# Performance work log

Hardware: AMD Instinct MI355X
Metric: run time of the kernel (lower is better)

The kernel has to match this reference:

```python
import jax, jax.numpy as jnp
import numpy as np

N_NODES = 50000
N_EDGES = 1_600_000
D = 256
H = 8
HD = D // H
EDGE_DIM = 32


def layer_norm(x, g, b, eps=1e-5):
    mu = jnp.mean(x, axis=-1, keepdims=True)
    var = jnp.var(x, axis=-1, keepdims=True)
    return (x - mu) * jax.lax.rsqrt(var + eps) * g + b


def setup_inputs() -> dict:
    key = jax.random.key(0)
    ks = jax.random.split(key, 24)
    def lin(k, out_d, in_d):
        s = 1.0 / np.sqrt(in_d)
        kw, kb = jax.random.split(k)
        W = jax.random.uniform(kw, (out_d, in_d), jnp.float32, -s, s)
        b = jax.random.uniform(kb, (out_d,), jnp.float32, -s, s)
        return W, b
    Wq, bq = lin(ks[0], D, D)
    Wk, bk = lin(ks[1], D, D)
    Wv, bv = lin(ks[2], D, D)
    We, be = lin(ks[3], HD, EDGE_DIM)
    Wo, bo = lin(ks[4], D, D)
    W1, b1 = lin(ks[5], 4 * D, D)
    W2, b2 = lin(ks[6], D, 4 * D)
    return {
        "x": jax.random.normal(ks[7], (N_NODES, D), jnp.float32),
        "edge_index": jax.random.randint(ks[8], (2, N_EDGES), 0, N_NODES, jnp.int64 if jax.config.jax_enable_x64 else jnp.int32),
        "edge_features": jax.random.normal(ks[9], (N_EDGES, EDGE_DIM), jnp.float32),
        "edge_weights": jax.random.uniform(ks[10], (N_EDGES,), jnp.float32),
        "Wq": Wq, "bq": bq, "Wk": Wk, "bk": bk, "Wv": Wv, "bv": bv,
        "We": We, "be": be, "Wo": Wo, "bo": bo,
        "W1": W1, "b1": b1, "W2": W2, "b2": b2,
        "g1": jnp.ones((D,), jnp.float32), "be1": jnp.zeros((D,), jnp.float32),
        "g2": jnp.ones((D,), jnp.float32), "be2": jnp.zeros((D,), jnp.float32),
        "alpha": jnp.ones((1,), jnp.float32), "beta": jnp.ones((1,), jnp.float32),
    }


def reference(x, edge_index, edge_features, edge_weights,
              Wq, bq, Wk, bk, Wv, bv, We, be, Wo, bo,
              W1, b1, W2, b2, g1, be1, g2, be2, alpha, beta):
    n = x.shape[0]
    scale = HD ** (-0.5)
    src, dst = edge_index[0], edge_index[1]

    # --- pre-norm + edge-aware attention ---
    xn = layer_norm(x, g1, be1)
    q = (xn @ Wq.T + bq).reshape(n, H, HD)
    k = (xn @ Wk.T + bk).reshape(n, H, HD)
    v = (xn @ Wv.T + bv).reshape(n, H, HD)
    ep = edge_features @ We.T + be  # [E, HD], shared across heads

    # per-edge scores: sum(q[dst] * (k[src] + ep)) * scale  -> [E, H]
    scores = jnp.einsum('ehd,ehd->eh', q[dst], k[src] + ep[:, None, :]) * scale
    scores = scores * edge_weights[:, None]

    # segment softmax over incoming edges of each dst node
    smax = jax.ops.segment_max(scores, dst, num_segments=n)  # [N, H]
    e = jnp.exp(scores - smax[dst])
    ssum = jax.ops.segment_sum(e, dst, num_segments=n)
    attn_weights = e / ssum[dst]  # [E, H]

    # gather-weighted scatter aggregate: [N, H, HD]
    agg = jax.ops.segment_sum(attn_weights[:, :, None] * v[src], dst, num_segments=n)
    attn_out = agg.reshape(n, D) @ Wo.T + bo  # dropout = identity (p=0)

    x = x + alpha * attn_out

    # --- feed-forward ---
    xn2 = layer_norm(x, g2, be2)
    ff = jax.nn.gelu(xn2 @ W1.T + b1, approximate=False) @ W2.T + b2
    x = x + beta * ff
    return x, attn_weights
```

## Files before the change

kernel.cpp:

```cpp
#include <hip/hip_runtime.h>

typedef short s16x8 __attribute__((ext_vector_type(8)));
typedef float f32x4 __attribute__((ext_vector_type(4)));

static constexpr int NN = 50000;
static constexpr int NE = 1600000;

__device__ __forceinline__ unsigned short f2b(float f) {
  union { float f; unsigned u; } c; c.f = f;
  unsigned x = c.u;
  x += 0x7fffu + ((x >> 16) & 1u);
  return (unsigned short)(x >> 16);
}
__device__ __forceinline__ int clampi(int v, int lo, int hi) {
  return v < lo ? lo : (v > hi ? hi : v);
}
__device__ __forceinline__ int rdl_i(int v, int l) {
  return __builtin_amdgcn_readlane(v, l);
}
__device__ __forceinline__ float rdl_f(float v, int l) {
  union { float f; int i; } c; c.f = v;
  c.i = __builtin_amdgcn_readlane(c.i, l);
  return c.f;
}

__global__ __launch_bounds__(256) void k_cvt(const float* __restrict__ s,
                                             unsigned short* __restrict__ d, int n) {
  const int i = blockIdx.x * 256 + threadIdx.x;
  if (i < n) d[i] = f2b(s[i]);
}

__global__ __launch_bounds__(256) void k_count(const int* __restrict__ dst,
                                               int* __restrict__ counts, int E) {
  const int e = blockIdx.x * 256 + threadIdx.x;
  if (e < E) atomicAdd(&counts[clampi(dst[e], 0, NN - 1)], 1);
}

__global__ __launch_bounds__(256) void k_reserve(const int* __restrict__ counts,
                                                 int* __restrict__ offs,
                                                 int* __restrict__ cursor,
                                                 int* __restrict__ counter, int n) {
  const int i = blockIdx.x * 256 + threadIdx.x;
  if (i >= n) return;
  const int c = counts[i];
  const int pos = atomicAdd(counter, c);
  offs[i] = pos;
  cursor[i] = pos;
}

__global__ __launch_bounds__(256) void k_scatter(const int* __restrict__ dst,
                                                 int* __restrict__ cursor,
                                                 int* __restrict__ sorted, int E) {
  const int e = blockIdx.x * 256 + threadIdx.x;
  if (e < E) {
    const int p = atomicAdd(&cursor[clampi(dst[e], 0, NN - 1)], 1);
    if (p >= 0 && p < E) sorted[p] = e;
  }
}

__global__ __launch_bounds__(256) void k_ln(const float* __restrict__ x,
                                            const float* __restrict__ g,
                                            const float* __restrict__ b,
                                            unsigned short* __restrict__ out, int n) {
  const int row = blockIdx.x * 4 + (threadIdx.x >> 6);
  if (row >= n) return;
  const int lane = threadIdx.x & 63;
  float4 xv = *(const float4*)(x + (size_t)row * 256 + 4 * lane);
  float v0 = xv.x, v1 = xv.y, v2 = xv.z, v3 = xv.w;
  float s = v0 + v1 + v2 + v3;
  float ss = v0 * v0 + v1 * v1 + v2 * v2 + v3 * v3;
#pragma unroll
  for (int m = 1; m < 64; m <<= 1) {
    s += __shfl_xor(s, m);
    ss += __shfl_xor(ss, m);
  }
  const float mu = s * (1.f / 256.f);
  const float var = ss * (1.f / 256.f) - mu * mu;
  const float rs = rsqrtf(var + 1e-5f);
  float4 gv = *(const float4*)(g + 4 * lane);
  float4 bv = *(const float4*)(b + 4 * lane);
  ushort4 o;
  o.x = f2b((v0 - mu) * rs * gv.x + bv.x);
  o.y = f2b((v1 - mu) * rs * gv.y + bv.y);
  o.z = f2b((v2 - mu) * rs * gv.z + bv.z);
  o.w = f2b((v3 - mu) * rs * gv.w + bv.w);
  *(ushort4*)(out + (size_t)row * 256 + 4 * lane) = o;
}

__global__ __launch_bounds__(256) void k_attn_score(
    const float* __restrict__ q, const float* __restrict__ k,
    const float* __restrict__ We, const float* __restrict__ be,
    const int* __restrict__ src, const float* __restrict__ ew,
    const float* __restrict__ ef, const int* __restrict__ offs,
    const int* __restrict__ counts, const int* __restrict__ sorted,
    float* __restrict__ scores, float* __restrict__ mxbuf) {
  __shared__ float WeS[32][36];
  __shared__ float beS[32];
  const int t = threadIdx.x;
  for (int i = t; i < 1024; i += 256) WeS[i >> 5][i & 31] = We[i];
  if (t < 32) beS[t] = be[t];
  __syncthreads();
  const int node = blockIdx.x * 4 + (t >> 6);
  if (node >= NN) return;
  const int lane = t & 63;
  const int h = lane >> 3;
  const int s8 = lane & 7;
  const float scale = 0.17677669529663689f;

  float4 qv = *(const float4*)(q + (size_t)node * 256 + 4 * lane);
  const float qarr[4] = {qv.x, qv.y, qv.z, qv.w};

  float w0 = 0.f, w1 = 0.f, w2 = 0.f, w3 = 0.f, qb = 0.f;
  const int d0 = 4 * s8;
#pragma unroll
  for (int t8 = 0; t8 < 8; ++t8) {
#pragma unroll
    for (int u = 0; u < 4; ++u) {
      const float qj = __shfl(qarr[u], 8 * h + t8);
      const int j = 4 * t8 + u;
      w0 += qj * WeS[j][d0 + 0];
      w1 += qj * WeS[j][d0 + 1];
      w2 += qj * WeS[j][d0 + 2];
      w3 += qj * WeS[j][d0 + 3];
      qb += qj * beS[j];
    }
  }

  const int beg = clampi(offs[node], 0, NE);
  const int cnt = clampi(counts[node], 0, NE - beg);

  float mx = -3.0e38f;
  for (int c = 0; c < cnt; c += 64) {
    const int ccnt = min(64, cnt - c);
    int eid_l = 0, s_l = 0;
    float ew_l = 0.f;
    if (lane < ccnt) {
      eid_l = clampi(sorted[beg + c + lane], 0, NE - 1);
      s_l = clampi(src[eid_l], 0, NN - 1);
      ew_l = ew[eid_l];
    }
    float4 kb0 = {0, 0, 0, 0}, kb1 = {0, 0, 0, 0};
    float4 eb0 = {0, 0, 0, 0}, eb1 = {0, 0, 0, 0};
    {
      const int s0 = rdl_i(s_l, 0), e0 = rdl_i(eid_l, 0);
      kb0 = *(const float4*)(k + (size_t)s0 * 256 + 4 * lane);
      eb0 = *(const float4*)(ef + (size_t)e0 * 32 + d0);
    }
    if (ccnt > 1) {
      const int s1 = rdl_i(s_l, 1), e1 = rdl_i(eid_l, 1);
      kb1 = *(const float4*)(k + (size_t)s1 * 256 + 4 * lane);
      eb1 = *(const float4*)(ef + (size_t)e1 * 32 + d0);
    }
    for (int j = 0; j < ccnt; ++j) {
      float4 kn = kb1, en = eb1;
      if (j + 2 < ccnt) {
        const int sn = rdl_i(s_l, j + 2), enid = rdl_i(eid_l, j + 2);
        kn = *(const float4*)(k + (size_t)sn * 256 + 4 * lane);
        en = *(const float4*)(ef + (size_t)enid * 32 + d0);
      }
      const float wgt = rdl_f(ew_l, j);
      const int eid = rdl_i(eid_l, j);
      float p = qv.x * kb0.x + qv.y * kb0.y + qv.z * kb0.z + qv.w * kb0.w +
                w0 * eb0.x + w1 * eb0.y + w2 * eb0.z + w3 * eb0.w;
      p += __shfl_xor(p, 1);
      p += __shfl_xor(p, 2);
      p += __shfl_xor(p, 4);
      const float scr = (p + qb) * scale * wgt;
      mx = fmaxf(mx, scr);
      if (s8 == 0) scores[(size_t)eid * 8 + h] = scr;
      kb0 = kb1; eb0 = eb1; kb1 = kn; eb1 = en;
    }
  }
  if (s8 == 0) mxbuf[(size_t)node * 8 + h] = mx;
}

__global__ __launch_bounds__(256) void k_attn_agg(
    const unsigned short* __restrict__ v, const int* __restrict__ src,
    const int* __restrict__ offs, const int* __restrict__ counts,
    const int* __restrict__ sorted, float* __restrict__ scores,
    const float* __restrict__ mxbuf, unsigned short* __restrict__ agg) {
  const int node = blockIdx.x * 4 + (threadIdx.x >> 6);
  if (node >= NN) return;
  const int lane = threadIdx.x & 63;
  const int h = lane >> 3;

  const int beg = clampi(offs[node], 0, NE);
  const int cnt = clampi(counts[node], 0, NE - beg);
  const int end = beg + cnt;
  const float mx = mxbuf[(size_t)node * 8 + h];

  float a0 = 0.f, a1 = 0.f, a2 = 0.f, a3 = 0.f, ssum = 0.f;
  for (int c = 0; c < cnt; c += 64) {
    const int ccnt = min(64, cnt - c);
    int eid_l = 0, s_l = 0;
    if (lane < ccnt) {
      eid_l = clampi(sorted[beg + c + lane], 0, NE - 1);
      s_l = clampi(src[eid_l], 0, NN - 1);
    }
    ushort4 vb0 = {0, 0, 0, 0}, vb1 = {0, 0, 0, 0};
    float sc0 = 0.f, sc1 = 0.f;
    {
      const int s0 = rdl_i(s_l, 0), e0 = rdl_i(eid_l, 0);
      vb0 = *(const ushort4*)(v + (size_t)s0 * 256 + 4 * lane);
      sc0 = scores[(size_t)e0 * 8 + h];
    }
    if (ccnt > 1) {
      const int s1 = rdl_i(s_l, 1), e1 = rdl_i(eid_l, 1);
      vb1 = *(const ushort4*)(v + (size_t)s1 * 256 + 4 * lane);
      sc1 = scores[(size_t)e1 * 8 + h];
    }
    for (int j = 0; j < ccnt; ++j) {
      ushort4 vn = vb1;
      float scn = sc1;
      if (j + 2 < ccnt) {
        const int sn = rdl_i(s_l, j + 2), enid = rdl_i(eid_l, j + 2);
        vn = *(const ushort4*)(v + (size_t)sn * 256 + 4 * lane);
        scn = scores[(size_t)enid * 8 + h];
      }
      const float e = __expf(sc0 - mx);
      ssum += e;
      union { unsigned u; float f; } c0, c1, c2, c3;
      c0.u = ((unsigned)vb0.x) << 16; c1.u = ((unsigned)vb0.y) << 16;
      c2.u = ((unsigned)vb0.z) << 16; c3.u = ((unsigned)vb0.w) << 16;
      a0 += e * c0.f; a1 += e * c1.f; a2 += e * c2.f; a3 += e * c3.f;
      vb0 = vb1; sc0 = sc1; vb1 = vn; sc1 = scn;
    }
  }
  const float inv = (cnt > 0) ? 1.f / ssum : 0.f;
  ushort4 o;
  o.x = f2b(a0 * inv); o.y = f2b(a1 * inv); o.z = f2b(a2 * inv); o.w = f2b(a3 * inv);
  *(ushort4*)(agg + (size_t)node * 256 + 4 * lane) = o;

  const float mxh = __shfl(mx, (lane & 7) * 8);
  const float invh = __shfl(inv, (lane & 7) * 8);
  for (int i2 = beg + (lane >> 3); i2 < end; i2 += 8) {
    const int eid = clampi(sorted[i2], 0, NE - 1);
    const size_t idx = (size_t)eid * 8 + (lane & 7);
    scores[idx] = __expf(scores[idx] - mxh) * invh;
  }
}

__global__ __launch_bounds__(256) void k_gemm(
    const unsigned short* __restrict__ A, const unsigned short* __restrict__ W,
    const float* __restrict__ bias, int M, int NC, int K, int epi,
    unsigned short* __restrict__ outb, float* __restrict__ outf,
    const float* __restrict__ resf, const float* __restrict__ scal) {
  const int lane = threadIdx.x & 63;
  const int wv = threadIdx.x >> 6;
  const int m0 = blockIdx.x * 64;
  const int c0 = blockIdx.y * 256 + wv * 64;
  const int r16 = lane & 15;
  const int quad = lane >> 4;

  f32x4 acc[4][4];
#pragma unroll
  for (int i = 0; i < 4; ++i)
#pragma unroll
    for (int j = 0; j < 4; ++j) acc[i][j] = {0.f, 0.f, 0.f, 0.f};

  int mclamp[4];
#pragma unroll
  for (int i = 0; i < 4; ++i) {
    int m = m0 + 16 * i + r16;
    mclamp[i] = (m < M) ? m : (M - 1);
  }

  for (int ko = 0; ko < K; ko += 32) {
    s16x8 a[4], b[4];
#pragma unroll
    for (int i = 0; i < 4; ++i)
      a[i] = *(const s16x8*)(A + (size_t)mclamp[i] * K + ko + quad * 8);
#pragma unroll
    for (int j = 0; j < 4; ++j)
      b[j] = *(const s16x8*)(W + (size_t)(c0 + 16 * j + r16) * K + ko + quad * 8);
#pragma unroll
    for (int i = 0; i < 4; ++i)
#pragma unroll
      for (int j = 0; j < 4; ++j)
        acc[i][j] = __builtin_amdgcn_mfma_f32_16x16x32_bf16(a[i], b[j], acc[i][j], 0, 0, 0);
  }

  const float sc = scal ? scal[0] : 0.f;
#pragma unroll
  for (int j = 0; j < 4; ++j) {
    const int c = c0 + 16 * j + r16;
    const float bc = bias[c];
#pragma unroll
    for (int i = 0; i < 4; ++i) {
#pragma unroll
      for (int r = 0; r < 4; ++r) {
        const int m = m0 + 16 * i + quad * 4 + r;
        if (m < M) {
          float f = acc[i][j][r] + bc;
          const size_t o = (size_t)m * NC + c;
          if (epi == 0) {
            outb[o] = f2b(f);
          } else if (epi == 1) {
            outf[o] = f;
          } else if (epi == 2) {
            outf[o] = resf[o] + sc * f;
          } else {
            outb[o] = f2b(0.5f * f * (1.f + erff(f * 0.70710678118654752f)));
          }
        }
      }
    }
  }
}

extern "C" void kernel_launch(void* const* d_in, const int* in_sizes, int n_in,
                              void* d_out, int out_size, void* d_ws, size_t ws_size,
                              hipStream_t stream) {
  (void)in_sizes; (void)n_in; (void)out_size; (void)ws_size;
  const float* x   = (const float*)d_in[0];
  const int* ei    = (const int*)d_in[1];
  const float* ef  = (const float*)d_in[2];
  const float* ew  = (const float*)d_in[3];
  const float* Wq  = (const float*)d_in[4];
  const float* bq  = (const float*)d_in[5];
  const float* Wk  = (const float*)d_in[6];
  const float* bk  = (const float*)d_in[7];
  const float* Wv  = (const float*)d_in[8];
  const float* bv  = (const float*)d_in[9];
  const float* We  = (const float*)d_in[10];
  const float* bel = (const float*)d_in[11];
  const float* Wo  = (const float*)d_in[12];
  const float* bo  = (const float*)d_in[13];
  const float* W1  = (const float*)d_in[14];
  const float* b1  = (const float*)d_in[15];
  const float* W2  = (const float*)d_in[16];
  const float* b2  = (const float*)d_in[17];
  const float* g1  = (const float*)d_in[18];
  const float* be1 = (const float*)d_in[19];
  const float* g2  = (const float*)d_in[20];
  const float* be2 = (const float*)d_in[21];
  const float* alpha = (const float*)d_in[22];
  const float* beta  = (const float*)d_in[23];

  char* w = (char*)d_ws;
  auto alloc = [&](size_t b) { char* p = w; w += (b + 255) & ~(size_t)255; return p; };

  int* counts          = (int*)alloc((size_t)(NN + 1) * 4);
  int* offs            = (int*)alloc((size_t)NN * 4);
  int* cursor          = (int*)alloc((size_t)NN * 4);
  int* sorted          = (int*)alloc((size_t)NE * 4);
  float* mxbuf         = (float*)alloc((size_t)NN * 8 * 4);
  unsigned short* wbf  = (unsigned short*)alloc((size_t)786432 * 2);
  unsigned short* xn   = (unsigned short*)alloc((size_t)NN * 256 * 2);
  float* qf            = (float*)alloc((size_t)NN * 256 * 4);
  float* kf            = (float*)alloc((size_t)NN * 256 * 4);
  unsigned short* vb   = (unsigned short*)alloc((size_t)NN * 256 * 2);

  unsigned short* wq_bf = wbf;
  unsigned short* wk_bf = wbf + 65536;
  unsigned short* wv_bf = wbf + 131072;
  unsigned short* wo_bf = wbf + 196608;
  unsigned short* w1_bf = wbf + 262144;
  unsigned short* w2_bf = wbf + 524288;

  unsigned short* agg = xn;
  unsigned short* xn2 = vb;
  unsigned short* h1  = (unsigned short*)qf;

  float* out_x   = (float*)d_out;
  float* scores  = (float*)d_out + (size_t)NN * 256;

  const int* src = ei;
  const int* dst = ei + NE;

  hipMemsetAsync(counts, 0, (size_t)(NN + 1) * 4, stream);
  k_count<<<dim3((NE + 255) / 256), dim3(256), 0, stream>>>(dst, counts, NE);
  k_reserve<<<dim3((NN + 255) / 256), dim3(256), 0, stream>>>(counts, offs, cursor, counts + NN, NN);
  k_scatter<<<dim3((NE + 255) / 256), dim3(256), 0, stream>>>(dst, cursor, sorted, NE);

  k_cvt<<<dim3(256), dim3(256), 0, stream>>>(Wq, wq_bf, 65536);
  k_cvt<<<dim3(256), dim3(256), 0, stream>>>(Wk, wk_bf, 65536);
  k_cvt<<<dim3(256), dim3(256), 0, stream>>>(Wv, wv_bf, 65536);
  k_cvt<<<dim3(256), dim3(256), 0, stream>>>(Wo, wo_bf, 65536);
  k_cvt<<<dim3(1024), dim3(256), 0, stream>>>(W1, w1_bf, 262144);
  k_cvt<<<dim3(1024), dim3(256), 0, stream>>>(W2, w2_bf, 262144);

  k_ln<<<dim3(NN / 4), dim3(256), 0, stream>>>(x, g1, be1, xn, NN);

  dim3 gB(256);
  dim3 g256((NN + 63) / 64, 1);
  k_gemm<<<g256, gB, 0, stream>>>(xn, wq_bf, bq, NN, 256, 256, 1, nullptr, qf, nullptr, nullptr);
  k_gemm<<<g256, gB, 0, stream>>>(xn, wk_bf, bk, NN, 256, 256, 1, nullptr, kf, nullptr, nullptr);
  k_gemm<<<g256, gB, 0, stream>>>(xn, wv_bf, bv, NN, 256, 256, 0, vb, nullptr, nullptr, nullptr);

  k_attn_score<<<dim3(NN / 4), dim3(256), 0, stream>>>(qf, kf, We, bel, src, ew, ef,
                                                       offs, counts, sorted, scores, mxbuf);
  k_attn_agg<<<dim3(NN / 4), dim3(256), 0, stream>>>(vb, src, offs, counts, sorted,
                                                     scores, mxbuf, agg);

  k_gemm<<<g256, gB, 0, stream>>>(agg, wo_bf, bo, NN, 256, 256, 2, nullptr, out_x, x, alpha);

  k_ln<<<dim3(NN / 4), dim3(256), 0, stream>>>(out_x, g2, be2, xn2, NN);

  dim3 g1024((NN + 63) / 64, 4);
  k_gemm<<<g1024, gB, 0, stream>>>(xn2, w1_bf, b1, NN, 1024, 256, 3, h1, nullptr, nullptr, nullptr);

  k_gemm<<<g256, gB, 0, stream>>>(h1, w2_bf, b2, NN, 256, 1024, 2, nullptr, out_x, out_x, beta);
}
```

Before: 1.705 ms.

## Fuse attention score and aggregation with online softmax; wave-level prefix in reserve

Merges the score and aggregation kernels into a single pass per destination node. It uses an online softmax that rescales the running sum and accumulators whenever a new maximum appears, so the max buffer and the second gather of edge lists, src indices and scores are no longer needed. The V rows are prefetched alongside K and edge features, which raises register pressure in the inner loop. Separately, the offset reservation now does a wave prefix scan with one atomic per wave instead of one atomic per node.

```diff
diff --git a/kernel.cpp b/kernel.cpp
--- a/kernel.cpp
+++ b/kernel.cpp
@@ -41,11 +41,23 @@
                                                  int* __restrict__ cursor,
                                                  int* __restrict__ counter, int n) {
   const int i = blockIdx.x * 256 + threadIdx.x;
-  if (i >= n) return;
-  const int c = counts[i];
-  const int pos = atomicAdd(counter, c);
-  offs[i] = pos;
-  cursor[i] = pos;
+  const int lane = threadIdx.x & 63;
+  const int c = (i < n) ? counts[i] : 0;
+  int pre = c;
+#pragma unroll
+  for (int m = 1; m < 64; m <<= 1) {
+    const int t = __shfl_up(pre, m);
+    if (lane >= m) pre += t;
+  }
+  const int wavesum = __shfl(pre, 63);
+  int base = 0;
+  if (lane == 0) base = atomicAdd(counter, wavesum);
+  base = __shfl(base, 0);
+  const int pos = base + pre - c;
+  if (i < n) {
+    offs[i] = pos;
+    cursor[i] = pos;
+  }
 }
 
 __global__ __launch_bounds__(256) void k_scatter(const int* __restrict__ dst,
@@ -87,13 +99,14 @@
   *(ushort4*)(out + (size_t)row * 256 + 4 * lane) = o;
 }
 
-__global__ __launch_bounds__(256) void k_attn_score(
+__global__ __launch_bounds__(256) void k_attn_fused(
     const float* __restrict__ q, const float* __restrict__ k,
+    const unsigned short* __restrict__ v,
     const float* __restrict__ We, const float* __restrict__ be,
     const int* __restrict__ src, const float* __restrict__ ew,
     const float* __restrict__ ef, const int* __restrict__ offs,
     const int* __restrict__ counts, const int* __restrict__ sorted,
-    float* __restrict__ scores, float* __restrict__ mxbuf) {
+    float* __restrict__ scores, unsigned short* __restrict__ agg) {
   __shared__ float WeS[32][36];
   __shared__ float beS[32];
   const int t = threadIdx.x;
@@ -105,13 +118,13 @@
   const int lane = t & 63;
   const int h = lane >> 3;
   const int s8 = lane & 7;
+  const int d0 = 4 * s8;
   const float scale = 0.17677669529663689f;
 
   float4 qv = *(const float4*)(q + (size_t)node * 256 + 4 * lane);
   const float qarr[4] = {qv.x, qv.y, qv.z, qv.w};
 
   float w0 = 0.f, w1 = 0.f, w2 = 0.f, w3 = 0.f, qb = 0.f;
-  const int d0 = 4 * s8;
 #pragma unroll
   for (int t8 = 0; t8 < 8; ++t8) {
 #pragma unroll
@@ -129,7 +142,9 @@
   const int beg = clampi(offs[node], 0, NE);
   const int cnt = clampi(counts[node], 0, NE - beg);
 
-  float mx = -3.0e38f;
+  float mx = -3.0e38f, ssum = 0.f;
+  float a0 = 0.f, a1 = 0.f, a2 = 0.f, a3 = 0.f;
+
   for (int c = 0; c < cnt; c += 64) {
     const int ccnt = min(64, cnt - c);
     int eid_l = 0, s_l = 0;
@@ -141,22 +156,27 @@
     }
     float4 kb0 = {0, 0, 0, 0}, kb1 = {0, 0, 0, 0};
     float4 eb0 = {0, 0, 0, 0}, eb1 = {0, 0, 0, 0};
+    ushort4 vb0 = {0, 0, 0, 0}, vb1 = {0, 0, 0, 0};
     {
       const int s0 = rdl_i(s_l, 0), e0 = rdl_i(eid_l, 0);
       kb0 = *(const float4*)(k + (size_t)s0 * 256 + 4 * lane);
       eb0 = *(const float4*)(ef + (size_t)e0 * 32 + d0);
+      vb0 = *(const ushort4*)(v + (size_t)s0 * 256 + 4 * lane);
     }
     if (ccnt > 1) {
       const int s1 = rdl_i(s_l, 1), e1 = rdl_i(eid_l, 1);
       kb1 = *(const float4*)(k + (size_t)s1 * 256 + 4 * lane);
       eb1 = *(const float4*)(ef + (size_t)e1 * 32 + d0);
+      vb1 = *(const ushort4*)(v + (size_t)s1 * 256 + 4 * lane);
     }
     for (int j = 0; j < ccnt; ++j) {
       float4 kn = kb1, en = eb1;
+      ushort4 vn = vb1;
       if (j + 2 < ccnt) {
         const int sn = rdl_i(s_l, j + 2), enid = rdl_i(eid_l, j + 2);
         kn = *(const float4*)(k + (size_t)sn * 256 + 4 * lane);
         en = *(const float4*)(ef + (size_t)enid * 32 + d0);
+        vn = *(const ushort4*)(v + (size_t)sn * 256 + 4 * lane);
       }
       const float wgt = rdl_f(ew_l, j);
       const int eid = rdl_i(eid_l, j);
@@ -166,64 +186,19 @@
       p += __shfl_xor(p, 2);
       p += __shfl_xor(p, 4);
       const float scr = (p + qb) * scale * wgt;
-      mx = fmaxf(mx, scr);
       if (s8 == 0) scores[(size_t)eid * 8 + h] = scr;
-      kb0 = kb1; eb0 = eb1; kb1 = kn; eb1 = en;
-    }
-  }
-  if (s8 == 0) mxbuf[(size_t)node * 8 + h] = mx;
-}
-
-__global__ __launch_bounds__(256) void k_attn_agg(
-    const unsigned short* __restrict__ v, const int* __restrict__ src,
-    const int* __restrict__ offs, const int* __restrict__ counts,
-    const int* __restrict__ sorted, float* __restrict__ scores,
-    const float* __restrict__ mxbuf, unsigned short* __restrict__ agg) {
-  const int node = blockIdx.x * 4 + (threadIdx.x >> 6);
-  if (node >= NN) return;
-  const int lane = threadIdx.x & 63;
-  const int h = lane >> 3;
-
-  const int beg = clampi(offs[node], 0, NE);
-  const int cnt = clampi(counts[node], 0, NE - beg);
-  const int end = beg + cnt;
-  const float mx = mxbuf[(size_t)node * 8 + h];
-
-  float a0 = 0.f, a1 = 0.f, a2 = 0.f, a3 = 0.f, ssum = 0.f;
-  for (int c = 0; c < cnt; c += 64) {
-    const int ccnt = min(64, cnt - c);
-    int eid_l = 0, s_l = 0;
-    if (lane < ccnt) {
-      eid_l = clampi(sorted[beg + c + lane], 0, NE - 1);
-      s_l = clampi(src[eid_l], 0, NN - 1);
-    }
-    ushort4 vb0 = {0, 0, 0, 0}, vb1 = {0, 0, 0, 0};
-    float sc0 = 0.f, sc1 = 0.f;
-    {
-      const int s0 = rdl_i(s_l, 0), e0 = rdl_i(eid_l, 0);
-      vb0 = *(const ushort4*)(v + (size_t)s0 * 256 + 4 * lane);
-      sc0 = scores[(size_t)e0 * 8 + h];
-    }
-    if (ccnt > 1) {
-      const int s1 = rdl_i(s_l, 1), e1 = rdl_i(eid_l, 1);
-      vb1 = *(const ushort4*)(v + (size_t)s1 * 256 + 4 * lane);
-      sc1 = scores[(size_t)e1 * 8 + h];
-    }
-    for (int j = 0; j < ccnt; ++j) {
-      ushort4 vn = vb1;
-      float scn = sc1;
-      if (j + 2 < ccnt) {
-        const int sn = rdl_i(s_l, j + 2), enid = rdl_i(eid_l, j + 2);
-        vn = *(const ushort4*)(v + (size_t)sn * 256 + 4 * lane);
-        scn = scores[(size_t)enid * 8 + h];
+      if (scr > mx) {
+        const float f = __expf(mx - scr);
+        ssum *= f; a0 *= f; a1 *= f; a2 *= f; a3 *= f;
+        mx = scr;
       }
-      const float e = __expf(sc0 - mx);
+      const float e = __expf(scr - mx);
       ssum += e;
       union { unsigned u; float f; } c0, c1, c2, c3;
       c0.u = ((unsigned)vb0.x) << 16; c1.u = ((unsigned)vb0.y) << 16;
       c2.u = ((unsigned)vb0.z) << 16; c3.u = ((unsigned)vb0.w) << 16;
       a0 += e * c0.f; a1 += e * c1.f; a2 += e * c2.f; a3 += e * c3.f;
-      vb0 = vb1; sc0 = sc1; vb1 = vn; sc1 = scn;
+      kb0 = kb1; eb0 = eb1; vb0 = vb1; kb1 = kn; eb1 = en; vb1 = vn;
     }
   }
   const float inv = (cnt > 0) ? 1.f / ssum : 0.f;
@@ -231,8 +206,11 @@
   o.x = f2b(a0 * inv); o.y = f2b(a1 * inv); o.z = f2b(a2 * inv); o.w = f2b(a3 * inv);
   *(ushort4*)(agg + (size_t)node * 256 + 4 * lane) = o;
 
+  __threadfence();
+
   const float mxh = __shfl(mx, (lane & 7) * 8);
   const float invh = __shfl(inv, (lane & 7) * 8);
+  const int end = beg + cnt;
   for (int i2 = beg + (lane >> 3); i2 < end; i2 += 8) {
     const int eid = clampi(sorted[i2], 0, NE - 1);
     const size_t idx = (size_t)eid * 8 + (lane & 7);
@@ -344,7 +322,6 @@
   int* offs            = (int*)alloc((size_t)NN * 4);
   int* cursor          = (int*)alloc((size_t)NN * 4);
   int* sorted          = (int*)alloc((size_t)NE * 4);
-  float* mxbuf         = (float*)alloc((size_t)NN * 8 * 4);
   unsigned short* wbf  = (unsigned short*)alloc((size_t)786432 * 2);
   unsigned short* xn   = (unsigned short*)alloc((size_t)NN * 256 * 2);
   float* qf            = (float*)alloc((size_t)NN * 256 * 4);
@@ -388,10 +365,8 @@
   k_gemm<<<g256, gB, 0, stream>>>(xn, wk_bf, bk, NN, 256, 256, 1, nullptr, kf, nullptr, nullptr);
   k_gemm<<<g256, gB, 0, stream>>>(xn, wv_bf, bv, NN, 256, 256, 0, vb, nullptr, nullptr, nullptr);
 
-  k_attn_score<<<dim3(NN / 4), dim3(256), 0, stream>>>(qf, kf, We, bel, src, ew, ef,
-                                                       offs, counts, sorted, scores, mxbuf);
-  k_attn_agg<<<dim3(NN / 4), dim3(256), 0, stream>>>(vb, src, offs, counts, sorted,
-                                                     scores, mxbuf, agg);
+  k_attn_fused<<<dim3(NN / 4), dim3(256), 0, stream>>>(qf, kf, vb, We, bel, src, ew, ef,
+                                                       offs, counts, sorted, scores, agg);
 
   k_gemm<<<g256, gB, 0, stream>>>(agg, wo_bf, bo, NN, 256, 256, 2, nullptr, out_x, x, alpha);
 
```

Result: slower. 3.783 ms (+121.9%).

## Stage GEMM tiles in LDS via global_load_lds and use 128x128 block tiles

Applied to the files above, without the earlier changes.

The GEMM kernel now copies 128x64 bf16 tiles of A and W into shared memory with direct global-to-LDS loads. All four waves then read their MFMA operands from LDS as a 2x2 arrangement of 64x64 sub-tiles, instead of each wave loading its own operands from global memory. This is meant to raise reuse of A and W across waves and cut global traffic, at the cost of LDS bank conflicts (the tiles are not padded), two barriers per K step, and a smaller grid. The CSR reserve kernel also switches to a wave-level prefix scan, so it issues one atomic per wave instead of one per node.

```diff
diff --git a/kernel.cpp b/kernel.cpp
--- a/kernel.cpp
+++ b/kernel.cpp
@@ -23,6 +23,10 @@
   c.i = __builtin_amdgcn_readlane(c.i, l);
   return c.f;
 }
+__device__ __forceinline__ void gl_lds16(const void* g, void* l) {
+  __builtin_amdgcn_global_load_lds((const __attribute__((address_space(1))) void*)g,
+                                   (__attribute__((address_space(3))) void*)l, 16, 0, 0);
+}
 
 __global__ __launch_bounds__(256) void k_cvt(const float* __restrict__ s,
                                              unsigned short* __restrict__ d, int n) {
@@ -41,11 +45,23 @@
                                                  int* __restrict__ cursor,
                                                  int* __restrict__ counter, int n) {
   const int i = blockIdx.x * 256 + threadIdx.x;
-  if (i >= n) return;
-  const int c = counts[i];
-  const int pos = atomicAdd(counter, c);
-  offs[i] = pos;
-  cursor[i] = pos;
+  const int lane = threadIdx.x & 63;
+  const int c = (i < n) ? counts[i] : 0;
+  int pre = c;
+#pragma unroll
+  for (int m = 1; m < 64; m <<= 1) {
+    const int t = __shfl_up(pre, m);
+    if (lane >= m) pre += t;
+  }
+  const int wavesum = __shfl(pre, 63);
+  int base = 0;
+  if (lane == 0) base = atomicAdd(counter, wavesum);
+  base = __shfl(base, 0);
+  const int pos = base + pre - c;
+  if (i < n) {
+    offs[i] = pos;
+    cursor[i] = pos;
+  }
 }
 
 __global__ __launch_bounds__(256) void k_scatter(const int* __restrict__ dst,
@@ -105,13 +121,13 @@
   const int lane = t & 63;
   const int h = lane >> 3;
   const int s8 = lane & 7;
+  const int d0 = 4 * s8;
   const float scale = 0.17677669529663689f;
 
   float4 qv = *(const float4*)(q + (size_t)node * 256 + 4 * lane);
   const float qarr[4] = {qv.x, qv.y, qv.z, qv.w};
 
   float w0 = 0.f, w1 = 0.f, w2 = 0.f, w3 = 0.f, qb = 0.f;
-  const int d0 = 4 * s8;
 #pragma unroll
   for (int t8 = 0; t8 < 8; ++t8) {
 #pragma unroll
@@ -245,10 +261,15 @@
     const float* __restrict__ bias, int M, int NC, int K, int epi,
     unsigned short* __restrict__ outb, float* __restrict__ outf,
     const float* __restrict__ resf, const float* __restrict__ scal) {
-  const int lane = threadIdx.x & 63;
-  const int wv = threadIdx.x >> 6;
-  const int m0 = blockIdx.x * 64;
-  const int c0 = blockIdx.y * 256 + wv * 64;
+  __shared__ unsigned short As[128 * 64];
+  __shared__ unsigned short Bs[128 * 64];
+  const int t = threadIdx.x;
+  const int lane = t & 63;
+  const int wv = t >> 6;
+  const int wr = wv >> 1;
+  const int wc = wv & 1;
+  const int m0 = blockIdx.x * 128;
+  const int c0 = blockIdx.y * 128;
   const int r16 = lane & 15;
   const int quad = lane >> 4;
 
@@ -258,38 +279,46 @@
 #pragma unroll
     for (int j = 0; j < 4; ++j) acc[i][j] = {0.f, 0.f, 0.f, 0.f};
 
-  int mclamp[4];
-#pragma unroll
-  for (int i = 0; i < 4; ++i) {
-    int m = m0 + 16 * i + r16;
-    mclamp[i] = (m < M) ? m : (M - 1);
-  }
-
-  for (int ko = 0; ko < K; ko += 32) {
-    s16x8 a[4], b[4];
-#pragma unroll
-    for (int i = 0; i < 4; ++i)
-      a[i] = *(const s16x8*)(A + (size_t)mclamp[i] * K + ko + quad * 8);
-#pragma unroll
-    for (int j = 0; j < 4; ++j)
-      b[j] = *(const s16x8*)(W + (size_t)(c0 + 16 * j + r16) * K + ko + quad * 8);
-#pragma unroll
-    for (int i = 0; i < 4; ++i)
+  for (int k0 = 0; k0 < K; k0 += 64) {
+#pragma unroll
+    for (int i = 0; i < 4; ++i) {
+      const int ob = wv * 1024 + i * 4096;
+      const int o = ob + lane * 16;
+      const int row = o >> 7;
+      const int colb = o & 127;
+      const int ra = (m0 + row < M) ? (m0 + row) : (M - 1);
+      gl_lds16((const char*)A + ((size_t)ra * K + k0) * 2 + colb, (char*)As + ob);
+      gl_lds16((const char*)W + ((size_t)(c0 + row) * K + k0) * 2 + colb, (char*)Bs + ob);
+    }
+    __syncthreads();
+#pragma unroll
+    for (int kk = 0; kk < 64; kk += 32) {
+      s16x8 a[4], b[4];
+#pragma unroll
+      for (int i = 0; i < 4; ++i)
+        a[i] = *(const s16x8*)(As + (wr * 64 + 16 * i + r16) * 64 + kk + quad * 8);
 #pragma unroll
       for (int j = 0; j < 4; ++j)
-        acc[i][j] = __builtin_amdgcn_mfma_f32_16x16x32_bf16(a[i], b[j], acc[i][j], 0, 0, 0);
+        b[j] = *(const s16x8*)(Bs + (wc * 64 + 16 * j + r16) * 64 + kk + quad * 8);
+#pragma unroll
+      for (int i = 0; i < 4; ++i)
+#pragma unroll
+        for (int j = 0; j < 4; ++j)
+          acc[i][j] = __builtin_amdgcn_mfma_f32_16x16x32_bf16(a[i], b[j], acc[i][j], 0, 0, 0);
+    }
+    __syncthreads();
   }
 
   const float sc = scal ? scal[0] : 0.f;
 #pragma unroll
   for (int j = 0; j < 4; ++j) {
-    const int c = c0 + 16 * j + r16;
+    const int c = c0 + wc * 64 + 16 * j + r16;
     const float bc = bias[c];
 #pragma unroll
     for (int i = 0; i < 4; ++i) {
 #pragma unroll
       for (int r = 0; r < 4; ++r) {
-        const int m = m0 + 16 * i + quad * 4 + r;
+        const int m = m0 + wr * 64 + 16 * i + quad * 4 + r;
         if (m < M) {
           float f = acc[i][j][r] + bc;
           const size_t o = (size_t)m * NC + c;
@@ -383,22 +412,22 @@
   k_ln<<<dim3(NN / 4), dim3(256), 0, stream>>>(x, g1, be1, xn, NN);
 
   dim3 gB(256);
-  dim3 g256((NN + 63) / 64, 1);
-  k_gemm<<<g256, gB, 0, stream>>>(xn, wq_bf, bq, NN, 256, 256, 1, nullptr, qf, nullptr, nullptr);
-  k_gemm<<<g256, gB, 0, stream>>>(xn, wk_bf, bk, NN, 256, 256, 1, nullptr, kf, nullptr, nullptr);
-  k_gemm<<<g256, gB, 0, stream>>>(xn, wv_bf, bv, NN, 256, 256, 0, vb, nullptr, nullptr, nullptr);
+  dim3 gQ((NN + 127) / 128, 2);
+  dim3 gF1((NN + 127) / 128, 8);
+  k_gemm<<<gQ, gB, 0, stream>>>(xn, wq_bf, bq, NN, 256, 256, 1, nullptr, qf, nullptr, nullptr);
+  k_gemm<<<gQ, gB, 0, stream>>>(xn, wk_bf, bk, NN, 256, 256, 1, nullptr, kf, nullptr, nullptr);
+  k_gemm<<<gQ, gB, 0, stream>>>(xn, wv_bf, bv, NN, 256, 256, 0, vb, nullptr, nullptr, nullptr);
 
   k_attn_score<<<dim3(NN / 4), dim3(256), 0, stream>>>(qf, kf, We, bel, src, ew, ef,
                                                        offs, counts, sorted, scores, mxbuf);
   k_attn_agg<<<dim3(NN / 4), dim3(256), 0, stream>>>(vb, src, offs, counts, sorted,
                                                      scores, mxbuf, agg);
 
-  k_gemm<<<g256, gB, 0, stream>>>(agg, wo_bf, bo, NN, 256, 256, 2, nullptr, out_x, x, alpha);
+  k_gemm<<<gQ, gB, 0, stream>>>(agg, wo_bf, bo, NN, 256, 256, 2, nullptr, out_x, x, alpha);
 
   k_ln<<<dim3(NN / 4), dim3(256), 0, stream>>>(out_x, g2, be2, xn2, NN);
 
-  dim3 g1024((NN + 63) / 64, 4);
-  k_gemm<<<g1024, gB, 0, stream>>>(xn2, w1_bf, b1, NN, 1024, 256, 3, h1, nullptr, nullptr, nullptr);
-
-  k_gemm<<<g256, gB, 0, stream>>>(h1, w2_bf, b2, NN, 256, 1024, 2, nullptr, out_x, out_x, beta);
-}
+  k_gemm<<<gF1, gB, 0, stream>>>(xn2, w1_bf, b1, NN, 1024, 256, 3, h1, nullptr, nullptr, nullptr);
+
+  k_gemm<<<gQ, gB, 0, stream>>>(h1, w2_bf, b2, NN, 256, 1024, 2, nullptr, out_x, out_x, beta);
+}
```

New measurement: 1.585 ms. 1.08x faster.
